# Kernel optimization log

Measured on AMD Instinct MI355X. Metric: run time of the kernel, lower is better.

## Reference

```python
import jax, jax.numpy as jnp
import numpy as np

NUM_CLASSES = 2   # module init num_classes; class logits have NUM_CLASSES+1 (incl. 'no object')
ORIG_H, ORIG_W = 512, 512  # original input resolution that masks are upsampled to


def setup_inputs() -> dict:
    key = jax.random.key(0)
    k1, k2 = jax.random.split(key)
    B, Q = 8, 100
    h, w = 128, 128  # mask decoder outputs at 1/4 input resolution
    class_queries_logits = jax.random.normal(k1, (B, Q, NUM_CLASSES + 1), dtype=jnp.float32)
    masks_queries_logits = jax.random.normal(k2, (B, Q, h, w), dtype=jnp.float32)
    return {"class_queries_logits": class_queries_logits,
            "masks_queries_logits": masks_queries_logits}


def reference(class_queries_logits, masks_queries_logits):
    B, Q = masks_queries_logits.shape[:2]
    # bilinear upsample to original resolution (align_corners=False == half-pixel centers)
    masks_up = jax.image.resize(masks_queries_logits, (B, Q, ORIG_H, ORIG_W), method="bilinear")
    # softmax over classes (incl. no-object), keep only the first NUM_CLASSES,
    # exactly as the original loop only indexes c in range(num_classes)
    class_probs = jax.nn.softmax(class_queries_logits, axis=-1)[..., :NUM_CLASSES]  # [B,Q,C]
    mask_probs = jax.nn.sigmoid(masks_up)  # [B,Q,H,W]
    # fused replacement for the triple b/q/c Python loop of weighted accumulates
    logits = jnp.einsum("bqc,bqhw->bchw", class_probs, mask_probs)  # [B,C,H,W]
    return logits
```

## Files before the change

kernel.cpp:

```cpp
#include <hip/hip_runtime.h>
#include <math.h>

#define NB 8
#define NQ 100
#define NQH 50
#define NCP1 3
#define NC 2
#define HIN 128
#define WIN 128
#define HOUT 512
#define WOUT 512
#define QSTR (HIN * WIN)
#define QBYTES (QSTR * 4)

#if __has_builtin(__builtin_amdgcn_exp2f)
#define EXP2F(x) __builtin_amdgcn_exp2f(x)
#else
#define EXP2F(x) exp2f(x)
#endif
#if __has_builtin(__builtin_amdgcn_rcpf)
#define RCPF(x) __builtin_amdgcn_rcpf(x)
#else
#define RCPF(x) (1.0f / (x))
#endif

__device__ __forceinline__ float bperm(int byteaddr, float v) {
  return __int_as_float(__builtin_amdgcn_ds_bpermute(byteaddr, __float_as_int(v)));
}

typedef float f32x4 __attribute__((ext_vector_type(4)));
typedef unsigned int u32x4 __attribute__((ext_vector_type(4)));

__global__ __launch_bounds__(512, 4)
void m2f_fused(const float* __restrict__ cls,
               const float* __restrict__ masks,
               float* __restrict__ out) {
  const int k   = blockIdx.x;
  const int b   = blockIdx.y;
  const int tid = threadIdx.x;

  __shared__ float  sigtab[4096];
  __shared__ float2 pq[NQ];
  __shared__ float  part[8][256];

#pragma unroll
  for (int j = 0; j < 8; ++j) {
    const int i = tid + j * 512;
    const float x = (float)i * 0.0078125f - 16.0f;
    sigtab[i] = RCPF(1.0f + EXP2F(x));
  }

  if (tid < NQ) {
    const float* cl = cls + (b * NQ + tid) * NCP1;
    float a0 = cl[0], a1 = cl[1], a2 = cl[2];
    float mx = fmaxf(a0, fmaxf(a1, a2));
    const float L2E = 1.4426950408889634f;
    float e0 = EXP2F((a0 - mx) * L2E);
    float e1 = EXP2F((a1 - mx) * L2E);
    float e2 = EXP2F((a2 - mx) * L2E);
    float inv = RCPF(e0 + e1 + e2);
    pq[tid] = make_float2(e0 * inv, e1 * inv);
  }
  __syncthreads();

  const int wave = tid >> 6;
  const int r    = wave & 3;
  const int qh   = wave >> 2;
  const int lane = tid & 63;
  const int q0   = qh * NQH;

  const int rlo = (r < 2) ? (k > 0 ? k - 1 : 0) : k;
  const int rhi = (r < 2) ? k : (k < HIN - 1 ? k + 1 : HIN - 1);
  const float NL2E128 = -1.4426950408889634f * 128.0f;
  const float wlo = ((r == 0) ? 0.375f : (r == 1) ? 0.125f
                   : (r == 2) ? 0.875f : 0.625f) * NL2E128;
  const float whi = ((r == 0) ? 0.625f : (r == 1) ? 0.875f
                   : (r == 2) ? 0.125f : 0.375f) * NL2E128;

  union { const float* p; unsigned long long u; } pn;
  pn.p = masks + (size_t)b * NQ * QSTR;
  u32x4 srd;
  srd.x = (unsigned int)pn.u;
  srd.y = (unsigned int)(pn.u >> 32) & 0xFFFFu;
  srd.z = (unsigned int)(NQ * QSTR * 4);
  srd.w = 0x00020000u;

  const int voffA = q0 * QBYTES + (rlo * WIN + 2 * lane) * 4;
  const int voffB = q0 * QBYTES + (rhi * WIN + 2 * lane) * 4;

  const int addrL = (lane - 1) << 2;
  const bool edgeL = (lane == 0);
  const bool edgeR = (lane == 63);

  float2 aS0 = make_float2(0.f, 0.f);
  float2 aSM = make_float2(0.f, 0.f);
  float2 aS1 = make_float2(0.f, 0.f);
  float2 aSR = make_float2(0.f, 0.f);

  f32x4 A0, B0, A1, B1, A2, B2, A3, B3, A4, B4;
  float sP0, sP1, sP2, sP3, sC0, sC1, sC2, sC3;

#define LOADSET(S, qrel)                                                  \
  do {                                                                    \
    asm volatile("buffer_load_dwordx4 %0, %2, %3, 0 offen\n\t"            \
                 "buffer_load_dwordx4 %1, %4, %3, 0 offen"                \
                 : "=&v"(A##S), "=&v"(B##S)                               \
                 : "v"(voffA + (qrel) * QBYTES), "s"(srd),                \
                   "v"(voffB + (qrel) * QBYTES));                         \
  } while (0)

#define WAITS(S)                                                          \
  asm volatile("s_waitcnt vmcnt(8)" : "+v"(A##S), "+v"(B##S))

#define SIG(u, sout)                                                      \
  do {                                                                    \
    float uc = fminf(fmaxf((u), 0.0f), 4095.0f);                          \
    sout = sigtab[(int)uc];                                               \
  } while (0)

#define GATHER(S)                                                         \
  do {                                                                    \
    float u0 = fmaf(wlo, A##S.x, fmaf(whi, B##S.x, 2048.5f));             \
    float u1 = fmaf(wlo, A##S.y, fmaf(whi, B##S.y, 2048.5f));             \
    float u2 = fmaf(wlo, A##S.z, fmaf(whi, B##S.z, 2048.5f));             \
    float um  = 0.5f * (u0 + u1);                                         \
    float umR = 0.5f * (u1 + u2);                                         \
    SIG(u0,  sC0);                                                        \
    SIG(um,  sC1);                                                        \
    SIG(u1,  sC2);                                                        \
    SIG(umR, sC3);                                                        \
  } while (0)

#define ACCROLL(qqprev)                                                   \
  do {                                                                    \
    const float2 pd = pq[qqprev];                                         \
    aS0.x = fmaf(pd.x, sP0, aS0.x);  aS0.y = fmaf(pd.y, sP0, aS0.y);      \
    aSM.x = fmaf(pd.x, sP1, aSM.x);  aSM.y = fmaf(pd.y, sP1, aSM.y);      \
    aS1.x = fmaf(pd.x, sP2, aS1.x);  aS1.y = fmaf(pd.y, sP2, aS1.y);      \
    aSR.x = fmaf(pd.x, sP3, aSR.x);  aSR.y = fmaf(pd.y, sP3, aSR.y);      \
    sP0 = sC0; sP1 = sC1; sP2 = sC2; sP3 = sC3;                           \
  } while (0)

#define PH(S, s)                                                          \
  do {                                                                    \
    WAITS(S);                                                             \
    GATHER(S);                                                            \
    LOADSET(S, (s) + 5);                                                  \
    ACCROLL(q0 + (s) - 1);                                                \
  } while (0)

  LOADSET(0, 0); LOADSET(1, 1); LOADSET(2, 2); LOADSET(3, 3); LOADSET(4, 4);

  WAITS(0);
  GATHER(0);
  sP0 = sC0; sP1 = sC1; sP2 = sC2; sP3 = sC3;
  LOADSET(0, 5);

  for (int q = 1; q < 41; q += 5) {
    PH(1, q);
    PH(2, q + 1);
    PH(3, q + 2);
    PH(4, q + 3);
    PH(0, q + 4);
  }
  PH(1, 41); PH(2, 42); PH(3, 43); PH(4, 44);

  asm volatile("s_waitcnt vmcnt(8)" : "+v"(A0), "+v"(B0));
  GATHER(0); ACCROLL(q0 + 44);
  asm volatile("s_waitcnt vmcnt(6)" : "+v"(A1), "+v"(B1));
  GATHER(1); ACCROLL(q0 + 45);
  asm volatile("s_waitcnt vmcnt(4)" : "+v"(A2), "+v"(B2));
  GATHER(2); ACCROLL(q0 + 46);
  asm volatile("s_waitcnt vmcnt(2)" : "+v"(A3), "+v"(B3));
  GATHER(3); ACCROLL(q0 + 47);
  asm volatile("s_waitcnt vmcnt(0)" : "+v"(A4), "+v"(B4));
  GATHER(4); ACCROLL(q0 + 48);
  {
    const float2 pd = pq[q0 + 49];
    aS0.x = fmaf(pd.x, sP0, aS0.x);  aS0.y = fmaf(pd.y, sP0, aS0.y);
    aSM.x = fmaf(pd.x, sP1, aSM.x);  aSM.y = fmaf(pd.y, sP1, aSM.y);
    aS1.x = fmaf(pd.x, sP2, aS1.x);  aS1.y = fmaf(pd.y, sP2, aS1.y);
    aSR.x = fmaf(pd.x, sP3, aSR.x);  aSR.y = fmaf(pd.y, sP3, aSR.y);
  }

  const int col = r * 64 + lane;
  if (qh == 1) {
    part[0][col] = aS0.x;  part[1][col] = aS0.y;
    part[2][col] = aSM.x;  part[3][col] = aSM.y;
    part[4][col] = aS1.x;  part[5][col] = aS1.y;
    part[6][col] = aSR.x;  part[7][col] = aSR.y;
  }
  __syncthreads();
  if (qh == 0) {
    aS0.x += part[0][col];  aS0.y += part[1][col];
    aSM.x += part[2][col];  aSM.y += part[3][col];
    aS1.x += part[4][col];  aS1.y += part[5][col];
    aSR.x += part[6][col];  aSR.y += part[7][col];

    float SLx_r = bperm(addrL, aSR.x);
    float SLy_r = bperm(addrL, aSR.y);
    float SLx = edgeL ? aS0.x : SLx_r;
    float SLy = edgeL ? aS0.y : SLy_r;
    float SRx = edgeR ? aS1.x : aSR.x;
    float SRy = edgeR ? aS1.y : aSR.y;

    float o0x = fmaf(0.25f, aS0.x, 0.75f * SLx);
    float o1x = fmaf(0.75f, aS0.x, 0.25f * SLx);
    float o2x = fmaf(0.25f, aSM.x, 0.75f * aS0.x);
    float o3x = fmaf(0.75f, aSM.x, 0.25f * aS0.x);
    float o4x = fmaf(0.25f, aS1.x, 0.75f * aSM.x);
    float o5x = fmaf(0.75f, aS1.x, 0.25f * aSM.x);
    float o6x = fmaf(0.25f, SRx,   0.75f * aS1.x);
    float o7x = fmaf(0.75f, SRx,   0.25f * aS1.x);
    float o0y = fmaf(0.25f, aS0.y, 0.75f * SLy);
    float o1y = fmaf(0.75f, aS0.y, 0.25f * SLy);
    float o2y = fmaf(0.25f, aSM.y, 0.75f * aS0.y);
    float o3y = fmaf(0.75f, aSM.y, 0.25f * aS0.y);
    float o4y = fmaf(0.25f, aS1.y, 0.75f * aSM.y);
    float o5y = fmaf(0.75f, aS1.y, 0.25f * aSM.y);
    float o6y = fmaf(0.25f, SRy,   0.75f * aS1.y);
    float o7y = fmaf(0.75f, SRy,   0.25f * aS1.y);

    const int y  = 4 * k + r;
    const int x0 = 8 * lane;
    float* o0 = out + (((size_t)b * NC + 0) * HOUT + y) * WOUT + x0;
    float* o1 = out + (((size_t)b * NC + 1) * HOUT + y) * WOUT + x0;
    *(float4*)o0       = make_float4(o0x, o1x, o2x, o3x);
    *(float4*)(o0 + 4) = make_float4(o4x, o5x, o6x, o7x);
    *(float4*)o1       = make_float4(o0y, o1y, o2y, o3y);
    *(float4*)(o1 + 4) = make_float4(o4y, o5y, o6y, o7y);
  }
}

extern "C" void kernel_launch(void* const* d_in, const int* in_sizes, int n_in,
                              void* d_out, int out_size, void* d_ws, size_t ws_size,
                              hipStream_t stream) {
  const float* cls   = (const float*)d_in[0];
  const float* masks = (const float*)d_in[1];
  float* out = (float*)d_out;
  dim3 grid(HIN, NB);
  m2f_fused<<<grid, 512, 0, stream>>>(cls, masks, out);
}
```

Before: 114.8 us.

## Deepen buffer-load prefetch ring to eight stages and swap grid axes

Raises the software-pipelined buffer_load ring from five to eight in-flight query slices per thread, adjusting the vmcnt waits and the drain sequence to match. It also swaps the grid dimensions so consecutive blocks run over batch rather than row index, which changes block scheduling order and cache locality. The deeper ring hides more memory latency but costs extra VGPRs (16 more f32x4 regs), which could cut occupancy under launch_bounds(512,4) or force spills.

```diff
diff --git a/kernel.cpp b/kernel.cpp
--- a/kernel.cpp
+++ b/kernel.cpp
@@ -35,8 +35,8 @@
 void m2f_fused(const float* __restrict__ cls,
                const float* __restrict__ masks,
                float* __restrict__ out) {
-  const int k   = blockIdx.x;
-  const int b   = blockIdx.y;
+  const int b   = blockIdx.x;
+  const int k   = blockIdx.y;
   const int tid = threadIdx.x;
 
   __shared__ float  sigtab[4096];
@@ -97,7 +97,7 @@
   float2 aS1 = make_float2(0.f, 0.f);
   float2 aSR = make_float2(0.f, 0.f);
 
-  f32x4 A0, B0, A1, B1, A2, B2, A3, B3, A4, B4;
+  f32x4 A0, B0, A1, B1, A2, B2, A3, B3, A4, B4, A5, B5, A6, B6, A7, B7;
   float sP0, sP1, sP2, sP3, sC0, sC1, sC2, sC3;
 
 #define LOADSET(S, qrel)                                                  \
@@ -109,8 +109,8 @@
                    "v"(voffB + (qrel) * QBYTES));                         \
   } while (0)
 
-#define WAITS(S)                                                          \
-  asm volatile("s_waitcnt vmcnt(8)" : "+v"(A##S), "+v"(B##S))
+#define WT(S, N)                                                          \
+  asm volatile("s_waitcnt vmcnt(" #N ")" : "+v"(A##S), "+v"(B##S))
 
 #define SIG(u, sout)                                                      \
   do {                                                                    \
@@ -143,38 +143,34 @@
 
 #define PH(S, s)                                                          \
   do {                                                                    \
-    WAITS(S);                                                             \
+    WT(S, 14);                                                            \
     GATHER(S);                                                            \
-    LOADSET(S, (s) + 5);                                                  \
+    LOADSET(S, (s) + 8);                                                  \
     ACCROLL(q0 + (s) - 1);                                                \
   } while (0)
 
-  LOADSET(0, 0); LOADSET(1, 1); LOADSET(2, 2); LOADSET(3, 3); LOADSET(4, 4);
-
-  WAITS(0);
+  LOADSET(0, 0); LOADSET(1, 1); LOADSET(2, 2); LOADSET(3, 3);
+  LOADSET(4, 4); LOADSET(5, 5); LOADSET(6, 6); LOADSET(7, 7);
+
+  WT(0, 14);
   GATHER(0);
   sP0 = sC0; sP1 = sC1; sP2 = sC2; sP3 = sC3;
-  LOADSET(0, 5);
-
-  for (int q = 1; q < 41; q += 5) {
-    PH(1, q);
-    PH(2, q + 1);
-    PH(3, q + 2);
-    PH(4, q + 3);
-    PH(0, q + 4);
-  }
-  PH(1, 41); PH(2, 42); PH(3, 43); PH(4, 44);
-
-  asm volatile("s_waitcnt vmcnt(8)" : "+v"(A0), "+v"(B0));
-  GATHER(0); ACCROLL(q0 + 44);
-  asm volatile("s_waitcnt vmcnt(6)" : "+v"(A1), "+v"(B1));
-  GATHER(1); ACCROLL(q0 + 45);
-  asm volatile("s_waitcnt vmcnt(4)" : "+v"(A2), "+v"(B2));
-  GATHER(2); ACCROLL(q0 + 46);
-  asm volatile("s_waitcnt vmcnt(2)" : "+v"(A3), "+v"(B3));
-  GATHER(3); ACCROLL(q0 + 47);
-  asm volatile("s_waitcnt vmcnt(0)" : "+v"(A4), "+v"(B4));
-  GATHER(4); ACCROLL(q0 + 48);
+  LOADSET(0, 8);
+
+  for (int q = 1; q < 41; q += 8) {
+    PH(1, q);     PH(2, q + 1); PH(3, q + 2); PH(4, q + 3);
+    PH(5, q + 4); PH(6, q + 5); PH(7, q + 6); PH(0, q + 7);
+  }
+  PH(1, 41);
+
+  WT(2, 14); GATHER(2); ACCROLL(q0 + 41);
+  WT(3, 12); GATHER(3); ACCROLL(q0 + 42);
+  WT(4, 10); GATHER(4); ACCROLL(q0 + 43);
+  WT(5, 8);  GATHER(5); ACCROLL(q0 + 44);
+  WT(6, 6);  GATHER(6); ACCROLL(q0 + 45);
+  WT(7, 4);  GATHER(7); ACCROLL(q0 + 46);
+  WT(0, 2);  GATHER(0); ACCROLL(q0 + 47);
+  WT(1, 0);  GATHER(1); ACCROLL(q0 + 48);
   {
     const float2 pd = pq[q0 + 49];
     aS0.x = fmaf(pd.x, sP0, aS0.x);  aS0.y = fmaf(pd.y, sP0, aS0.y);
@@ -238,6 +234,6 @@
   const float* cls   = (const float*)d_in[0];
   const float* masks = (const float*)d_in[1];
   float* out = (float*)d_out;
-  dim3 grid(HIN, NB);
+  dim3 grid(NB, HIN);
   m2f_fused<<<grid, 512, 0, stream>>>(cls, masks, out);
 }
```

Measured after the change: 118.8 us. +3.4%, slower.
